# Optimization experiments

Measured on AMD Instinct MI355X. Metric: run time of the kernel, lower is better.

## Reference

```python
import math
import jax, jax.numpy as jnp
import numpy as np

HID = 4096      # hidden_size
NH = 32         # num_attention_heads
HD = HID // NH  # head_dim = 128
EDGE = 24       # image_edge
K = 12          # pool_kernel_size
PE = 1 + EDGE - K  # pooled_edge = 13
VT = EDGE * EDGE   # vision_tokens = 576
OFF = 5         # image token offset
SR = 2          # scale_ratio


def setup_inputs() -> dict:
    key = jax.random.key(0)
    k1, k2, k3 = jax.random.split(key, 3)
    B, S = 2, 1024
    hidden_states = jax.random.normal(k1, (B, S, HID), jnp.float32)
    W_in = jax.random.normal(k2, (HID, HID), jnp.float32) * 0.02   # input_proj.weight [out,in]
    W_up = jax.random.normal(k3, (HD * SR * SR, HD), jnp.float32) * 0.02  # up_proj.weight [out,in]
    return {"hidden_states": hidden_states, "W_in": W_in, "W_up": W_up}


def reference(hidden_states, W_in, W_up):
    B, S, _ = hidden_states.shape
    residual = hidden_states
    # [B, NH, S, HD] (q and k are identical views of hidden_states)
    qk = hidden_states.reshape(B, S, NH, HD).transpose(0, 2, 1, 3)
    attn = jnp.einsum('bhqd,bhkd->bhqk', qk, qk) / math.sqrt(HD)
    # additive mask applied along the QUERY dim (faithful to original broadcast)
    mask = jnp.zeros((S,), attn.dtype).at[OFF:OFF + VT].set(jnp.finfo(attn.dtype).min)
    attn = attn + mask[None, None, :, None]
    attn = jax.nn.softmax(attn.astype(jnp.float32), axis=-1).astype(qk.dtype)
    attn = attn.sum(axis=2)                        # [B, NH, S]
    image_attn = attn[:, :, OFF:OFF + VT]          # [B, NH, 576]
    image_states = qk[:, :, OFF:OFF + VT, :].reshape(B, NH, EDGE, EDGE, HD)
    ia_soft = jax.nn.softmax(image_attn, axis=-1).reshape(B, NH, EDGE, EDGE)
    ia = image_attn.reshape(B, NH, EDGE, EDGE)
    # AvgPool2d(kernel=12, stride=1) -> [B, NH, 13, 13]
    pooled = jax.lax.reduce_window(ia, 0.0, jax.lax.add,
                                   (1, 1, K, K), (1, 1, 1, 1), 'VALID') / (K * K)
    idx = jnp.argmax(pooled.reshape(B, NH, -1), axis=-1)   # [B, NH]
    row = idx // PE
    col = idx % PE

    def per_head(sm, st, r, c):
        w = jax.lax.dynamic_slice(sm, (r, c), (K, K)).sum()
        win = jax.lax.dynamic_slice(st, (r, c, 0), (K, K, HD))
        return w, win

    # vmap over batch and heads; traced dynamic-slice starts replace the python loops
    w, win = jax.vmap(jax.vmap(per_head))(ia_soft, image_states, row, col)
    up = jnp.einsum('bhijd,ed->bhije', win, W_up)
    # pixel-shuffle back to 24x24 (transpose(3,4) in torch view order)
    up = up.reshape(B, NH, K, K, SR, SR, HD).transpose(0, 1, 2, 4, 3, 5, 6)
    up = up.reshape(B, NH, VT, HD) * w[:, :, None, None]
    img = up.transpose(0, 2, 1, 3).reshape(B, VT, HID)
    hs = jnp.concatenate([hidden_states[:, :OFF], img, hidden_states[:, OFF + VT:]], axis=1)
    hs = jax.nn.silu(hs @ W_in.T)
    return residual + hs
```

## Files before the change

kernel.cpp:

```cpp
#include <hip/hip_runtime.h>
#include <hip/hip_bf16.h>
#include <math.h>

#define HID 4096
#define NH 32
#define HD 128
#define EDGE 24
#define KW 12
#define PEW 13
#define VT 576
#define OFF 5
#define NB 2
#define SLEN 1024
#define QT 64
#define NQT 7
#define KT 64
#define NKT 16
#define NSB 448
#define NWB 128

typedef short bf16x8 __attribute__((ext_vector_type(8)));
typedef float f32x4 __attribute__((ext_vector_type(4)));
typedef unsigned int u32;

static __device__ __forceinline__ unsigned short f2bf(float f) {
  union { float f; u32 u; } v; v.f = f;
  u32 u = v.u;
  return (unsigned short)((u + 0x7fffu + ((u >> 16) & 1u)) >> 16);
}

static __device__ __forceinline__ float dot4(float4 a, float4 b) {
  return a.x * b.x + a.y * b.y + a.z * b.z + a.w * b.w;
}

static __device__ __forceinline__ void load_lds16(const void* g, void* l) {
  __builtin_amdgcn_global_load_lds((const __attribute__((address_space(1))) u32*)g,
                                   (__attribute__((address_space(3))) u32*)l, 16, 0, 0);
}

__global__ __launch_bounds__(256) void k_prep(const float* __restrict__ hid,
                                              unsigned short* __restrict__ Phi,
                                              unsigned short* __restrict__ Plo) {
  const int STR = 2048 * 256;
  int t0 = blockIdx.x * 256 + threadIdx.x;
  for (int i = t0; i < NB * SLEN * HID / 4; i += STR) {
    float4 x = ((const float4*)hid)[i];
    float e[4] = {x.x, x.y, x.z, x.w};
    ushort4 hv, lv;
    unsigned short* hp = (unsigned short*)&hv;
    unsigned short* lp = (unsigned short*)&lv;
#pragma unroll
    for (int j = 0; j < 4; ++j) {
      u32 u = __float_as_uint(e[j]);
      u32 hb = (u + 0x7fffu + ((u >> 16) & 1u)) >> 16;
      float r = e[j] - __uint_as_float(hb << 16);
      u32 ur = __float_as_uint(r);
      u32 lb = (ur + 0x7fffu + ((ur >> 16) & 1u)) >> 16;
      hp[j] = (unsigned short)hb;
      lp[j] = (unsigned short)lb;
    }
    ((ushort4*)Phi)[i] = hv;
    ((ushort4*)Plo)[i] = lv;
  }
}

__global__ __launch_bounds__(512, 2) void k_scores(const unsigned short* __restrict__ Phi,
                                                   const unsigned short* __restrict__ Plo,
                                                   float* __restrict__ part,
                                                   const float* __restrict__ Win,
                                                   unsigned short* __restrict__ Wb) {
  __shared__ unsigned short Kh[3][KT * HD];
  __shared__ float cs[4][SLEN];
  __shared__ float zbuf[2][QT];

  int bid = blockIdx.x;
  int t = threadIdx.x;

  if (bid >= NSB) {
    int base = (bid - NSB) * 32768;
#pragma unroll 4
    for (int it = 0; it < 64; ++it) {
      int i = base + it * 512 + t;
      float4 v = ((const float4*)Win)[i];
      ushort4 o;
      o.x = f2bf(v.x); o.y = f2bf(v.y); o.z = f2bf(v.z); o.w = f2bf(v.w);
      ((ushort4*)Wb)[i] = o;
    }
    return;
  }

  int xcd = bid & 7, idx = bid >> 3;
  int bh = xcd * 8 + idx / NQT;
  int qt = idx % NQT;
  int b = bh >> 5, h = bh & 31;
  int l = t & 63, wv = t >> 6;
  int wq = wv >> 1, wk = wv & 1;

  const unsigned short* PhB = Phi + (size_t)b * SLEN * HID + h * HD;
  const unsigned short* PlB = Plo + (size_t)b * SLEN * HID + h * HD;

  bf16x8 qhi[4], qlo[4];
  {
    int ql = qt * QT + wq * 16 + (l & 15);
    int qg = (ql < OFF) ? ql : ql + VT;
    const unsigned short* ph = PhB + (size_t)qg * HID + (l >> 4) * 8;
    const unsigned short* pl = PlB + (size_t)qg * HID + (l >> 4) * 8;
#pragma unroll
    for (int ds = 0; ds < 4; ++ds) {
      qhi[ds] = *(const bf16x8*)(ph + ds * 32);
      qlo[ds] = *(const bf16x8*)(pl + ds * 32);
    }
  }

  int g0 = t, g1 = t + 512;
  int r0 = g0 >> 4, r1 = g1 >> 4;
  size_t soff0 = (size_t)r0 * HID + ((g0 & 15) ^ (r0 & 7)) * 8;
  size_t soff1 = (size_t)r1 * HID + ((g1 & 15) ^ (r1 & 7)) * 8;

#define STAGE(kt_, bb_)                                                        \
  do {                                                                         \
    size_t kb_ = (size_t)(kt_)*KT * HID;                                       \
    load_lds16(PhB + kb_ + soff0, &Kh[bb_][g0 * 8]);                           \
    load_lds16(PhB + kb_ + soff1, &Kh[bb_][g1 * 8]);                           \
  } while (0)

  const float scale = 0.088388347648318447f;

  int foff[2][4];
#pragma unroll
  for (int c = 0; c < 2; ++c) {
    int rb = wk * 32 + c * 16 + (l & 15);
#pragma unroll
    for (int ds = 0; ds < 4; ++ds)
      foff[c][ds] = rb * HD + (((ds * 4) + (l >> 4)) ^ (rb & 7)) * 8;
  }

  float e[NKT][2][4];

  STAGE(0, 0);
  STAGE(1, 1);

#pragma unroll
  for (int tt = 0; tt < NKT; ++tt) {
    int bb = tt % 3;
    if (tt < NKT - 1) {
      asm volatile("s_waitcnt vmcnt(2)" ::: "memory");
    } else {
      asm volatile("s_waitcnt vmcnt(0)" ::: "memory");
    }
    __builtin_amdgcn_s_barrier();
    __builtin_amdgcn_sched_barrier(0);

    bf16x8 kh[2][4];
#pragma unroll
    for (int c = 0; c < 2; ++c)
#pragma unroll
      for (int ds = 0; ds < 4; ++ds)
        kh[c][ds] = *(const bf16x8*)&Kh[bb][foff[c][ds]];
    if (tt + 2 < NKT) STAGE(tt + 2, (tt + 2) % 3);

#pragma unroll
    for (int c = 0; c < 2; ++c) {
      f32x4 aP = {0.f, 0.f, 0.f, 0.f};
      f32x4 aR = {0.f, 0.f, 0.f, 0.f};
#pragma unroll
      for (int ds = 0; ds < 4; ++ds) {
        aP = __builtin_amdgcn_mfma_f32_16x16x32_bf16(qhi[ds], kh[c][ds], aP, 0, 0, 0);
        aR = __builtin_amdgcn_mfma_f32_16x16x32_bf16(qlo[ds], kh[c][ds], aR, 0, 0, 0);
      }
#pragma unroll
      for (int jj = 0; jj < 4; ++jj)
        e[tt][c][jj] = __expf((aP[jj] + aR[jj]) * scale);
    }
  }
#undef STAGE

  float zr[4] = {0.f, 0.f, 0.f, 0.f};
#pragma unroll
  for (int tt = 0; tt < NKT; ++tt)
#pragma unroll
    for (int c = 0; c < 2; ++c)
#pragma unroll
      for (int jj = 0; jj < 4; ++jj) zr[jj] += e[tt][c][jj];
#pragma unroll
  for (int jj = 0; jj < 4; ++jj) {
    float z = zr[jj];
    z += __shfl_xor(z, 1);
    z += __shfl_xor(z, 2);
    z += __shfl_xor(z, 4);
    z += __shfl_xor(z, 8);
    zr[jj] = z;
  }
  if ((l & 15) == 0) {
#pragma unroll
    for (int jj = 0; jj < 4; ++jj)
      zbuf[wk][wq * 16 + (l >> 4) * 4 + jj] = zr[jj];
  }
  __syncthreads();

  float zinv[4];
#pragma unroll
  for (int jj = 0; jj < 4; ++jj) {
    int row = wq * 16 + (l >> 4) * 4 + jj;
    zinv[jj] = 1.f / (zbuf[0][row] + zbuf[1][row]);
  }

#pragma unroll
  for (int tt = 0; tt < NKT; ++tt)
#pragma unroll
    for (int c = 0; c < 2; ++c) {
      float v = e[tt][c][0] * zinv[0] + e[tt][c][1] * zinv[1] +
                e[tt][c][2] * zinv[2] + e[tt][c][3] * zinv[3];
      v += __shfl_xor(v, 16);
      v += __shfl_xor(v, 32);
      if (l < 16) cs[wq][tt * KT + wk * 32 + c * 16 + l] = v;
    }
  __syncthreads();

  for (int c5 = t; c5 < VT; c5 += 512) {
    int col = OFF + c5;
    part[((size_t)bh * NQT + qt) * VT + c5] =
        (cs[0][col] + cs[1][col]) + (cs[2][col] + cs[3][col]);
  }
}

__global__ __launch_bounds__(256) void k_head(const float* __restrict__ part,
                                              float* __restrict__ params) {
  int bh = blockIdx.x;
  int t = threadIdx.x;
  __shared__ float ia[VT];
  __shared__ float sfe[VT];
  __shared__ float rbuf[256];
  __shared__ int ribuf[256];

  for (int i = t; i < VT; i += 256) {
    float s = 0.f;
    const float* p = part + (size_t)bh * NQT * VT + i;
    for (int c = 0; c < NQT; ++c) s += p[(size_t)c * VT];
    ia[i] = s;
  }
  __syncthreads();

  float lm = -1e30f;
  for (int i = t; i < VT; i += 256) lm = fmaxf(lm, ia[i]);
  rbuf[t] = lm;
  __syncthreads();
  for (int s = 128; s > 0; s >>= 1) {
    if (t < s) rbuf[t] = fmaxf(rbuf[t], rbuf[t + s]);
    __syncthreads();
  }
  float M = rbuf[0];
  __syncthreads();

  float lz = 0.f;
  for (int i = t; i < VT; i += 256) {
    float e = __expf(ia[i] - M);
    sfe[i] = e;
    lz += e;
  }
  rbuf[t] = lz;
  __syncthreads();
  for (int s = 128; s > 0; s >>= 1) {
    if (t < s) rbuf[t] += rbuf[t + s];
    __syncthreads();
  }
  float invZ = 1.f / rbuf[0];
  __syncthreads();

  float pv = -1e30f;
  int pidx = 0x7fffffff;
  if (t < PEW * PEW) {
    int r = t / PEW, c = t % PEW;
    float s = 0.f;
    for (int i = 0; i < KW; ++i)
      for (int j = 0; j < KW; ++j) s += ia[(r + i) * EDGE + (c + j)];
    pv = s;
    pidx = t;
  }
  rbuf[t] = pv;
  ribuf[t] = pidx;
  __syncthreads();
  for (int s = 128; s > 0; s >>= 1) {
    if (t < s) {
      float ov = rbuf[t + s];
      int oi = ribuf[t + s];
      if (ov > rbuf[t] || (ov == rbuf[t] && oi < ribuf[t])) {
        rbuf[t] = ov;
        ribuf[t] = oi;
      }
    }
    __syncthreads();
  }
  int idx = ribuf[0];
  int r0 = idx / PEW, c0 = idx % PEW;
  __syncthreads();

  float lw = 0.f;
  if (t < KW * KW) {
    int i = t / KW, j = t % KW;
    lw = sfe[(r0 + i) * EDGE + (c0 + j)];
  }
  rbuf[t] = lw;
  __syncthreads();
  for (int s = 128; s > 0; s >>= 1) {
    if (t < s) rbuf[t] += rbuf[t + s];
    __syncthreads();
  }
  if (t == 0) {
    params[bh * 4 + 0] = rbuf[0] * invZ;
    ((int*)params)[bh * 4 + 1] = r0;
    ((int*)params)[bh * 4 + 2] = c0;
  }
}

__global__ __launch_bounds__(256) void k_img(const float* __restrict__ hid,
                                             const float* __restrict__ Wup,
                                             const float* __restrict__ params,
                                             unsigned short* __restrict__ hs) {
  int bid = blockIdx.x;
  int g = bid & 3;
  int bh = bid >> 2;
  int b = bh / NH, h = bh % NH;
  float w = params[bh * 4];
  int r0 = ((const int*)params)[bh * 4 + 1];
  int c0 = ((const int*)params)[bh * 4 + 2];
  int t = threadIdx.x;

  __shared__ float win[36][HD];
  for (int idx = t; idx < 36 * (HD / 4); idx += 256) {
    int cell = idx >> 5;
    int c4 = idx & 31;
    int cc = g * 36 + cell;
    int i = cc / 12, j = cc % 12;
    int s = OFF + (r0 + i) * EDGE + (c0 + j);
    *(float4*)&win[cell][c4 * 4] =
        *(const float4*)(hid + ((size_t)(b * SLEN + s)) * HID + h * HD + c4 * 4);
  }
  __syncthreads();

  float acc0[36], acc1[36];
#pragma unroll
  for (int cell = 0; cell < 36; ++cell) { acc0[cell] = 0.f; acc1[cell] = 0.f; }

  int e0 = t, e1 = t + 256;
  const float* w0 = Wup + (size_t)e0 * HD;
  const float* w1 = Wup + (size_t)e1 * HD;
  for (int c = 0; c < 32; ++c) {
    float4 u0 = *(const float4*)(w0 + c * 4);
    float4 u1 = *(const float4*)(w1 + c * 4);
#pragma unroll
    for (int cell = 0; cell < 36; ++cell) {
      float4 qv = *(const float4*)&win[cell][c * 4];
      acc0[cell] += dot4(qv, u0);
      acc1[cell] += dot4(qv, u1);
    }
  }

  int si0 = e0 >> 8, sj0 = (e0 >> 7) & 1, d0 = e0 & 127;
  int si1 = e1 >> 8, sj1 = (e1 >> 7) & 1, d1 = e1 & 127;
#pragma unroll
  for (int cell = 0; cell < 36; ++cell) {
    int cc = g * 36 + cell;
    int i = cc / 12, j = cc % 12;
    {
      int srow = OFF + (2 * i + si0) * EDGE + (2 * j + sj0);
      hs[((size_t)(b * SLEN + srow)) * HID + h * HD + d0] = f2bf(acc0[cell] * w);
    }
    {
      int srow = OFF + (2 * i + si1) * EDGE + (2 * j + sj1);
      hs[((size_t)(b * SLEN + srow)) * HID + h * HD + d1] = f2bf(acc1[cell] * w);
    }
  }
}

__global__ __launch_bounds__(512, 2) void k_gemm(const unsigned short* __restrict__ A,
                                                 const unsigned short* __restrict__ Bm,
                                                 const float* __restrict__ resid,
                                                 float* __restrict__ out) {
  __shared__ unsigned short lA[3][128 * 64];
  __shared__ unsigned short lB[3][256 * 64];

  int bid0 = blockIdx.x;
  int swz = (bid0 & 7) * 32 + (bid0 >> 3);
  int bm0 = (swz & 15) << 7;
  int bn0 = (swz >> 4) << 8;
  int t = threadIdx.x;
  int ln = t & 63, wv = t >> 6;
  int wr = wv >> 2, wc = wv & 3;

  int aOff[4][2], bOff[4][2];
#pragma unroll
  for (int q = 0; q < 4; ++q)
#pragma unroll
    for (int ks = 0; ks < 2; ++ks) {
      int ga = ks * 4 + (ln >> 4);
      int ra = wr * 64 + q * 16 + (ln & 15);
      aOff[q][ks] = ra * 64 + ((ga ^ (ra & 7)) * 8);
      int rb = wc * 64 + q * 16 + (ln & 15);
      bOff[q][ks] = rb * 64 + ((ga ^ (rb & 7)) * 8);
    }

  const unsigned short* aS0; const unsigned short* aS1;
  unsigned short *aD0, *aD1;
  {
    int G = t, r = G >> 3, g = G & 7;
    aS0 = A + (size_t)(bm0 + r) * HID + ((g ^ (r & 7)) * 8);
    aD0 = &lA[0][0] + G * 8;
    G = t + 512; r = G >> 3; g = G & 7;
    aS1 = A + (size_t)(bm0 + r) * HID + ((g ^ (r & 7)) * 8);
    aD1 = &lA[0][0] + G * 8;
  }
  const unsigned short *bS0, *bS1, *bS2, *bS3;
  unsigned short *bD0, *bD1, *bD2, *bD3;
  {
    int G = t, r = G >> 3, g = G & 7;
    bS0 = Bm + (size_t)(bn0 + r) * HID + ((g ^ (r & 7)) * 8);
    bD0 = &lB[0][0] + G * 8;
    G = t + 512; r = G >> 3; g = G & 7;
    bS1 = Bm + (size_t)(bn0 + r) * HID + ((g ^ (r & 7)) * 8);
    bD1 = &lB[0][0] + G * 8;
    G = t + 1024; r = G >> 3; g = G & 7;
    bS2 = Bm + (size_t)(bn0 + r) * HID + ((g ^ (r & 7)) * 8);
    bD2 = &lB[0][0] + G * 8;
    G = t + 1536; r = G >> 3; g = G & 7;
    bS3 = Bm + (size_t)(bn0 + r) * HID + ((g ^ (r & 7)) * 8);
    bD3 = &lB[0][0] + G * 8;
  }

#define STAGE_ALL(kt_, nb_)                                \
  load_lds16(aS0 + (kt_) * 64, aD0 + (nb_) * 8192);        \
  load_lds16(aS1 + (kt_) * 64, aD1 + (nb_) * 8192);        \
  load_lds16(bS0 + (kt_) * 64, bD0 + (nb_) * 16384);       \
  load_lds16(bS1 + (kt_) * 64, bD1 + (nb_) * 16384);       \
  load_lds16(bS2 + (kt_) * 64, bD2 + (nb_) * 16384);       \
  load_lds16(bS3 + (kt_) * 64, bD3 + (nb_) * 16384);

  f32x4 acc[4][4];
#pragma unroll
  for (int mi = 0; mi < 4; ++mi)
#pragma unroll
    for (int ni = 0; ni < 4; ++ni) acc[mi][ni] = (f32x4){0.f, 0.f, 0.f, 0.f};

  STAGE_ALL(0, 0);
  STAGE_ALL(1, 1);

  int cur = 0;
  for (int kt = 0; kt < 64; ++kt) {
    if (kt < 63) {
      asm volatile("s_waitcnt vmcnt(6)" ::: "memory");
    } else {
      asm volatile("s_waitcnt vmcnt(0)" ::: "memory");
    }
    __builtin_amdgcn_s_barrier();

    const unsigned short* Ab = &lA[0][0] + cur * 8192;
    const unsigned short* Bb = &lB[0][0] + cur * 16384;

    bf16x8 aF[4][2], bF[4][2];
#pragma unroll
    for (int q = 0; q < 4; ++q) {
      aF[q][0] = *(const bf16x8*)(Ab + aOff[q][0]);
      aF[q][1] = *(const bf16x8*)(Ab + aOff[q][1]);
      bF[q][0] = *(const bf16x8*)(Bb + bOff[q][0]);
      bF[q][1] = *(const bf16x8*)(Bb + bOff[q][1]);
    }

    int nb = cur + 2; if (nb >= 3) nb -= 3;
    if (kt < 62) { STAGE_ALL(kt + 2, nb); }

    __builtin_amdgcn_s_setprio(1);
#pragma unroll
    for (int ni = 0; ni < 4; ++ni)
#pragma unroll
      for (int mi = 0; mi < 4; ++mi) {
        acc[mi][ni] = __builtin_amdgcn_mfma_f32_16x16x32_bf16(aF[mi][0], bF[ni][0],
                                                              acc[mi][ni], 0, 0, 0);
        acc[mi][ni] = __builtin_amdgcn_mfma_f32_16x16x32_bf16(aF[mi][1], bF[ni][1],
                                                              acc[mi][ni], 0, 0, 0);
      }
    __builtin_amdgcn_s_setprio(0);

    cur = cur + 1; if (cur >= 3) cur = 0;
  }
#undef STAGE_ALL

#pragma unroll
  for (int mi = 0; mi < 4; ++mi) {
#pragma unroll
    for (int ni = 0; ni < 4; ++ni) {
      int m = bm0 + wr * 64 + mi * 16 + (ln >> 4) * 4;
      int n = bn0 + wc * 64 + ni * 16 + (ln & 15);
#pragma unroll
      for (int r = 0; r < 4; ++r) {
        float x = acc[mi][ni][r];
        float s = x / (1.f + __expf(-x));
        size_t o = (size_t)(m + r) * HID + n;
        out[o] = resid[o] + s;
      }
    }
  }
}

extern "C" void kernel_launch(void* const* d_in, const int* in_sizes, int n_in,
                              void* d_out, int out_size, void* d_ws, size_t ws_size,
                              hipStream_t stream) {
  const float* hid = (const float*)d_in[0];
  const float* Win = (const float*)d_in[1];
  const float* Wup = (const float*)d_in[2];
  float* out = (float*)d_out;
  char* ws = (char*)d_ws;

  unsigned short* Wb  = (unsigned short*)ws;
  unsigned short* Phi = (unsigned short*)(ws + 33554432);
  float* part = (float*)(ws + 50331648);
  float* params = (float*)(ws + 52396032);
  unsigned short* Plo = (unsigned short*)d_out;

  k_prep<<<2048, 256, 0, stream>>>(hid, Phi, Plo);
  k_scores<<<NSB + NWB, 512, 0, stream>>>(Phi, Plo, part, Win, Wb);
  k_head<<<NB * NH, 256, 0, stream>>>(part, params);
  k_img<<<NB * NH * 4, 256, 0, stream>>>(hid, Wup, params, Phi);
  k_gemm<<<256, 512, 0, stream>>>(Phi, Wb, hid, out);
}
```

Baseline: 177.1 us.

## Recompute attention scores in two passes to drop register array; fuse head and image kernels

The scores kernel no longer keeps all 128 exp values per thread in registers. It computes the row normaliser in a first pass over the keys, then recomputes the MFMA scores in a second pass to form the column sums, and raises the launch-bounds occupancy hint from 2 to 4 blocks. The per-head argmax kernel is merged into the image-window kernel, so each of the 4 blocks per head redoes the pooling and argmax itself, which removes one launch and the params round trip. The prep kernel also skips writing low-order bf16 parts for image rows that the scores kernel never reads as queries. The cost is twice the MFMA and K-tile loads in the scores kernel, plus redundant head computation across blocks.

Measured after the change: 178.1 us. Within noise of the previous version (+0.6%).

```diff
diff --git a/kernel.cpp b/kernel.cpp
--- a/kernel.cpp
+++ b/kernel.cpp
@@ -60,11 +60,12 @@
       lp[j] = (unsigned short)lb;
     }
     ((ushort4*)Phi)[i] = hv;
-    ((ushort4*)Plo)[i] = lv;
-  }
-}
-
-__global__ __launch_bounds__(512, 2) void k_scores(const unsigned short* __restrict__ Phi,
+    int s = (i >> 10) & (SLEN - 1);
+    if (s < OFF || s >= OFF + VT) ((ushort4*)Plo)[i] = lv;
+  }
+}
+
+__global__ __launch_bounds__(512, 4) void k_scores(const unsigned short* __restrict__ Phi,
                                                    const unsigned short* __restrict__ Plo,
                                                    float* __restrict__ part,
                                                    const float* __restrict__ Win,
@@ -113,9 +114,9 @@
   }
 
   int g0 = t, g1 = t + 512;
-  int r0 = g0 >> 4, r1 = g1 >> 4;
-  size_t soff0 = (size_t)r0 * HID + ((g0 & 15) ^ (r0 & 7)) * 8;
-  size_t soff1 = (size_t)r1 * HID + ((g1 & 15) ^ (r1 & 7)) * 8;
+  int r0g = g0 >> 4, r1g = g1 >> 4;
+  size_t soff0 = (size_t)r0g * HID + ((g0 & 15) ^ (r0g & 7)) * 8;
+  size_t soff1 = (size_t)r1g * HID + ((g1 & 15) ^ (r1g & 7)) * 8;
 
 #define STAGE(kt_, bb_)                                                        \
   do {                                                                         \
@@ -135,19 +136,15 @@
       foff[c][ds] = rb * HD + (((ds * 4) + (l >> 4)) ^ (rb & 7)) * 8;
   }
 
-  float e[NKT][2][4];
+  float zacc[4] = {0.f, 0.f, 0.f, 0.f};
+  float zinv[4];
 
   STAGE(0, 0);
   STAGE(1, 1);
 
-#pragma unroll
   for (int tt = 0; tt < NKT; ++tt) {
     int bb = tt % 3;
-    if (tt < NKT - 1) {
-      asm volatile("s_waitcnt vmcnt(2)" ::: "memory");
-    } else {
-      asm volatile("s_waitcnt vmcnt(0)" ::: "memory");
-    }
+    asm volatile("s_waitcnt vmcnt(2)" ::: "memory");
     __builtin_amdgcn_s_barrier();
     __builtin_amdgcn_sched_barrier(0);
 
@@ -157,7 +154,7 @@
 #pragma unroll
       for (int ds = 0; ds < 4; ++ds)
         kh[c][ds] = *(const bf16x8*)&Kh[bb][foff[c][ds]];
-    if (tt + 2 < NKT) STAGE(tt + 2, (tt + 2) % 3);
+    STAGE((tt + 2) & (NKT - 1), (tt + 2) % 3);
 
 #pragma unroll
     for (int c = 0; c < 2; ++c) {
@@ -170,51 +167,69 @@
       }
 #pragma unroll
       for (int jj = 0; jj < 4; ++jj)
-        e[tt][c][jj] = __expf((aP[jj] + aR[jj]) * scale);
-    }
-  }
-#undef STAGE
-
-  float zr[4] = {0.f, 0.f, 0.f, 0.f};
-#pragma unroll
-  for (int tt = 0; tt < NKT; ++tt)
-#pragma unroll
-    for (int c = 0; c < 2; ++c)
-#pragma unroll
-      for (int jj = 0; jj < 4; ++jj) zr[jj] += e[tt][c][jj];
+        zacc[jj] += __expf((aP[jj] + aR[jj]) * scale);
+    }
+  }
+
 #pragma unroll
   for (int jj = 0; jj < 4; ++jj) {
-    float z = zr[jj];
+    float z = zacc[jj];
     z += __shfl_xor(z, 1);
     z += __shfl_xor(z, 2);
     z += __shfl_xor(z, 4);
     z += __shfl_xor(z, 8);
-    zr[jj] = z;
+    zacc[jj] = z;
   }
   if ((l & 15) == 0) {
 #pragma unroll
     for (int jj = 0; jj < 4; ++jj)
-      zbuf[wk][wq * 16 + (l >> 4) * 4 + jj] = zr[jj];
-  }
-  __syncthreads();
-
-  float zinv[4];
+      zbuf[wk][wq * 16 + (l >> 4) * 4 + jj] = zacc[jj];
+  }
+  __syncthreads();
 #pragma unroll
   for (int jj = 0; jj < 4; ++jj) {
     int row = wq * 16 + (l >> 4) * 4 + jj;
     zinv[jj] = 1.f / (zbuf[0][row] + zbuf[1][row]);
   }
 
-#pragma unroll
-  for (int tt = 0; tt < NKT; ++tt)
+  for (int tt = NKT; tt < 2 * NKT; ++tt) {
+    int kt = tt & (NKT - 1);
+    int bb = tt % 3;
+    if (tt < 2 * NKT - 1) {
+      asm volatile("s_waitcnt vmcnt(2)" ::: "memory");
+    } else {
+      asm volatile("s_waitcnt vmcnt(0)" ::: "memory");
+    }
+    __builtin_amdgcn_s_barrier();
+    __builtin_amdgcn_sched_barrier(0);
+
+    bf16x8 kh[2][4];
+#pragma unroll
+    for (int c = 0; c < 2; ++c)
+#pragma unroll
+      for (int ds = 0; ds < 4; ++ds)
+        kh[c][ds] = *(const bf16x8*)&Kh[bb][foff[c][ds]];
+    if (tt + 2 < 2 * NKT) STAGE((tt + 2) & (NKT - 1), (tt + 2) % 3);
+
 #pragma unroll
     for (int c = 0; c < 2; ++c) {
-      float v = e[tt][c][0] * zinv[0] + e[tt][c][1] * zinv[1] +
-                e[tt][c][2] * zinv[2] + e[tt][c][3] * zinv[3];
+      f32x4 aP = {0.f, 0.f, 0.f, 0.f};
+      f32x4 aR = {0.f, 0.f, 0.f, 0.f};
+#pragma unroll
+      for (int ds = 0; ds < 4; ++ds) {
+        aP = __builtin_amdgcn_mfma_f32_16x16x32_bf16(qhi[ds], kh[c][ds], aP, 0, 0, 0);
+        aR = __builtin_amdgcn_mfma_f32_16x16x32_bf16(qlo[ds], kh[c][ds], aR, 0, 0, 0);
+      }
+      float v = __expf((aP[0] + aR[0]) * scale) * zinv[0] +
+                __expf((aP[1] + aR[1]) * scale) * zinv[1] +
+                __expf((aP[2] + aR[2]) * scale) * zinv[2] +
+                __expf((aP[3] + aR[3]) * scale) * zinv[3];
       v += __shfl_xor(v, 16);
       v += __shfl_xor(v, 32);
-      if (l < 16) cs[wq][tt * KT + wk * 32 + c * 16 + l] = v;
-    }
+      if (l < 16) cs[wq][kt * KT + wk * 32 + c * 16 + l] = v;
+    }
+  }
+#undef STAGE
   __syncthreads();
 
   for (int c5 = t; c5 < VT; c5 += 512) {
@@ -224,14 +239,21 @@
   }
 }
 
-__global__ __launch_bounds__(256) void k_head(const float* __restrict__ part,
-                                              float* __restrict__ params) {
-  int bh = blockIdx.x;
+__global__ __launch_bounds__(256) void k_himg(const float* __restrict__ part,
+                                              const float* __restrict__ hid,
+                                              const float* __restrict__ Wup,
+                                              unsigned short* __restrict__ hs) {
+  int bid = blockIdx.x;
+  int g = bid & 3;
+  int bh = bid >> 2;
+  int b = bh / NH, h = bh % NH;
   int t = threadIdx.x;
+
   __shared__ float ia[VT];
   __shared__ float sfe[VT];
   __shared__ float rbuf[256];
   __shared__ int ribuf[256];
+  __shared__ float win[36][HD];
 
   for (int i = t; i < VT; i += 256) {
     float s = 0.f;
@@ -306,30 +328,12 @@
     if (t < s) rbuf[t] += rbuf[t + s];
     __syncthreads();
   }
-  if (t == 0) {
-    params[bh * 4 + 0] = rbuf[0] * invZ;
-    ((int*)params)[bh * 4 + 1] = r0;
-    ((int*)params)[bh * 4 + 2] = c0;
-  }
-}
-
-__global__ __launch_bounds__(256) void k_img(const float* __restrict__ hid,
-                                             const float* __restrict__ Wup,
-                                             const float* __restrict__ params,
-                                             unsigned short* __restrict__ hs) {
-  int bid = blockIdx.x;
-  int g = bid & 3;
-  int bh = bid >> 2;
-  int b = bh / NH, h = bh % NH;
-  float w = params[bh * 4];
-  int r0 = ((const int*)params)[bh * 4 + 1];
-  int c0 = ((const int*)params)[bh * 4 + 2];
-  int t = threadIdx.x;
-
-  __shared__ float win[36][HD];
-  for (int idx = t; idx < 36 * (HD / 4); idx += 256) {
-    int cell = idx >> 5;
-    int c4 = idx & 31;
+  float w = rbuf[0] * invZ;
+  __syncthreads();
+
+  for (int idx2 = t; idx2 < 36 * (HD / 4); idx2 += 256) {
+    int cell = idx2 >> 5;
+    int c4 = idx2 & 31;
     int cc = g * 36 + cell;
     int i = cc / 12, j = cc % 12;
     int s = OFF + (r0 + i) * EDGE + (c0 + j);
@@ -513,12 +517,10 @@
   unsigned short* Wb  = (unsigned short*)ws;
   unsigned short* Phi = (unsigned short*)(ws + 33554432);
   float* part = (float*)(ws + 50331648);
-  float* params = (float*)(ws + 52396032);
   unsigned short* Plo = (unsigned short*)d_out;
 
   k_prep<<<2048, 256, 0, stream>>>(hid, Phi, Plo);
   k_scores<<<NSB + NWB, 512, 0, stream>>>(Phi, Plo, part, Win, Wb);
-  k_head<<<NB * NH, 256, 0, stream>>>(part, params);
-  k_img<<<NB * NH * 4, 256, 0, stream>>>(hid, Wup, params, Phi);
+  k_himg<<<NB * NH * 4, 256, 0, stream>>>(part, hid, Wup, Phi);
   k_gemm<<<256, 512, 0, stream>>>(Phi, Wb, hid, out);
 }
```
